# Kernel tuning notes

Hardware: AMD Instinct MI355X
Metric: run time of the kernel (lower is better)

## Reference

```python
import jax, jax.numpy as jnp
import numpy as np

T, B, V, E, H, L = 128, 32, 50000, 512, 512, 2


def _lstm_layer(x, h0, c0, Wih, Whh, bih, bhh):
    # x: [T, B, in]; torch gate order i, f, g, o
    def step(carry, xt):
        h, c = carry
        gates = xt @ Wih.T + bih + h @ Whh.T + bhh  # [B, 4H]
        i, f, g, o = jnp.split(gates, 4, axis=-1)
        c = jax.nn.sigmoid(f) * c + jax.nn.sigmoid(i) * jnp.tanh(g)
        h = jax.nn.sigmoid(o) * jnp.tanh(c)
        return (h, c), h
    (h, c), ys = jax.lax.scan(step, (h0, c0), x)
    return ys, h, c


def setup_inputs() -> dict:
    key = jax.random.key(0)
    ks = jax.random.split(key, 12)
    s = 0.02
    return {
        'word': jax.random.randint(ks[0], (B,), 0, V),
        'seq': jax.random.randint(ks[1], (T, B), 0, V),
        'emb': jax.random.normal(ks[2], (V, E), jnp.float32) * s,
        'w2h_W': jax.random.normal(ks[3], (H, E), jnp.float32) * s,
        'w2h_b': jnp.zeros((H,), jnp.float32),
        'Wih0': jax.random.normal(ks[4], (4 * H, E), jnp.float32) * s,
        'Whh0': jax.random.normal(ks[5], (4 * H, H), jnp.float32) * s,
        'bih0': jnp.zeros((4 * H,), jnp.float32),
        'bhh0': jnp.zeros((4 * H,), jnp.float32),
        'Wih1': jax.random.normal(ks[6], (4 * H, H), jnp.float32) * s,
        'Whh1': jax.random.normal(ks[7], (4 * H, H), jnp.float32) * s,
        'bih1': jnp.zeros((4 * H,), jnp.float32),
        'bhh1': jnp.zeros((4 * H,), jnp.float32),
        'dec_W': jax.random.normal(ks[8], (V, H), jnp.float32) * s,
        'dec_b': jnp.zeros((V,), jnp.float32),
    }


def reference(word, seq, emb, w2h_W, w2h_b, Wih0, Whh0, bih0, bhh0,
              Wih1, Whh1, bih1, bhh1, dec_W, dec_b):
    word_emb = emb[word]                       # [B, E]
    seq_emb = emb[seq]                         # [T, B, E] (dropouts are 0/eval)
    # init_hidden: c0 = word2hidden(word_emb) expanded to all layers, h0 = 0
    c0 = word_emb @ w2h_W.T + w2h_b            # [B, H]
    h0 = jnp.zeros_like(c0)
    # 2-layer LSTM; stepping all layers per timestep == running layers sequentially
    y0, h_f0, c_f0 = _lstm_layer(seq_emb, h0, c0, Wih0, Whh0, bih0, bhh0)
    y1, h_f1, c_f1 = _lstm_layer(y0, h0, c0, Wih1, Whh1, bih1, bhh1)
    out = y1.reshape(T * B, H)                 # [T*B, H]
    decoded = out @ dec_W.T + dec_b            # [T*B, V]
    h_final = jnp.stack([h_f0, h_f1], axis=0)  # [L, B, H]
    c_final = jnp.stack([c_f0, c_f1], axis=0)
    return decoded, h_final, c_final
```

## Files before the change

### kernel.cpp

```cpp
#include <hip/hip_runtime.h>
#include <hip/hip_bf16.h>
#include <cstdint>

#define T_STEPS 128
#define BATCH   32
#define VOCAB   50000
#define EDIM    512
#define HDIM    512
#define GDIM    2048
#define MROWS   4096
#define VPAD    50048

typedef short bf16x8 __attribute__((ext_vector_type(8)));
typedef float f32x4  __attribute__((ext_vector_type(4)));
typedef unsigned short us4 __attribute__((ext_vector_type(4)));
typedef unsigned short us8 __attribute__((ext_vector_type(8)));

#define MFMA16(a, b, c) __builtin_amdgcn_mfma_f32_16x16x32_bf16(a, b, c, 0, 0, 0)

__device__ __forceinline__ float fsigmoid(float x) {
    return 1.0f / (1.0f + __expf(-x));
}
__device__ __forceinline__ float ftanh(float x) {
    return 1.0f - 2.0f / (1.0f + __expf(2.0f * x));
}

__device__ __forceinline__ unsigned short f2bf(float f) {
    unsigned int u = __float_as_uint(f);
    u = (u + 0x7fffu + ((u >> 16) & 1u)) >> 16;
    return (unsigned short)u;
}


__global__ __launch_bounds__(256) void conv_decw(const float* __restrict__ src,
                                                 unsigned short* __restrict__ dst) {
    long i = ((long)blockIdx.x * 256 + threadIdx.x) * 8;
    if (i >= (long)VPAD * EDIM) return;
    long row = i >> 9;
    us8 v;
    if (row < VOCAB) {
        float4 a = *(const float4*)(src + i);
        float4 b = *(const float4*)(src + i + 4);
        v[0] = f2bf(a.x); v[1] = f2bf(a.y); v[2] = f2bf(a.z); v[3] = f2bf(a.w);
        v[4] = f2bf(b.x); v[5] = f2bf(b.y); v[6] = f2bf(b.z); v[7] = f2bf(b.w);
    } else {
        v = (us8)0;
    }
    *(us8*)(dst + i) = v;
}

__global__ __launch_bounds__(64) void pack_conv(const float* __restrict__ src,
                                                unsigned short* __restrict__ dst) {
    const int n = blockIdx.x;
    const int orig = (n & 3) * 512 + (n >> 2);
    const int k = threadIdx.x * 8;
    const float* s = src + (long)orig * 512 + k;
    float4 a = *(const float4*)s;
    float4 b = *(const float4*)(s + 4);
    us8 v;
    v[0] = f2bf(a.x); v[1] = f2bf(a.y); v[2] = f2bf(a.z); v[3] = f2bf(a.w);
    v[4] = f2bf(b.x); v[5] = f2bf(b.y); v[6] = f2bf(b.z); v[7] = f2bf(b.w);
    *(us8*)(dst + (long)n * 512 + k) = v;
}

__global__ __launch_bounds__(256) void pack_bias(const float* __restrict__ bih0,
                                                 const float* __restrict__ bhh0,
                                                 const float* __restrict__ bih1,
                                                 const float* __restrict__ bhh1,
                                                 float* __restrict__ b0p,
                                                 float* __restrict__ b1p) {
    const int n = blockIdx.x * 256 + threadIdx.x;
    const int orig = (n & 3) * 512 + (n >> 2);
    b0p[n] = bih0[orig] + bhh0[orig];
    b1p[n] = bih1[orig] + bhh1[orig];
}

__global__ __launch_bounds__(256) void gather_x(const int* __restrict__ seq,
                                                const float* __restrict__ emb,
                                                unsigned short* __restrict__ Xbf) {
    long i = ((long)blockIdx.x * 256 + threadIdx.x) * 4;
    if (i >= (long)MROWS * EDIM) return;
    int r   = (int)(i >> 9);
    int col = (int)(i & 511);
    const float* er = emb + (long)seq[r] * EDIM + col;
    float4 e = *(const float4*)er;
    us4 v;
    v[0] = f2bf(e.x); v[1] = f2bf(e.y); v[2] = f2bf(e.z); v[3] = f2bf(e.w);
    *(us4*)(Xbf + i) = v;
}

__global__ __launch_bounds__(256) void init_c0(const int* __restrict__ word,
                                               const float* __restrict__ emb,
                                               const float* __restrict__ w2hW,
                                               const float* __restrict__ w2hb,
                                               float* __restrict__ c0s, float* __restrict__ c1s,
                                               unsigned short* __restrict__ h0A,
                                               unsigned short* __restrict__ h1A) {
    const int idx = blockIdx.x * 256 + threadIdx.x;
    const int b = idx >> 9, hh = idx & 511;
    const float* er = emb + (long)word[b] * EDIM;
    const float* wr = w2hW + (long)hh * EDIM;
    float acc = w2hb[hh];
    #pragma unroll 4
    for (int k = 0; k < EDIM; k += 4) {
        float4 e4 = *(const float4*)(er + k);
        float4 w4 = *(const float4*)(wr + k);
        acc += e4.x * w4.x + e4.y * w4.y + e4.z * w4.z + e4.w * w4.w;
    }
    c0s[idx] = acc;
    c1s[idx] = acc;
    h0A[idx] = 0;
    h1A[idx] = 0;
}

__global__ __launch_bounds__(256) void gemm_bt128(const unsigned short* __restrict__ A,
                                                  const unsigned short* __restrict__ Bt,
                                                  float* __restrict__ C,
                                                  const float* __restrict__ bias1,
                                                  const float* __restrict__ bias2,
                                                  int K, int Nreal, long ldc, int ntn,
                                                  int mode) {
    __shared__ __align__(16) unsigned short As[128 * 64];
    __shared__ __align__(16) unsigned short Bs[128 * 64];
    const int tid  = threadIdx.x;
    long m0, n0;
    if (mode & 2) {
        m0 = (long)(blockIdx.x & 31) * 128;
        n0 = (long)(blockIdx.x >> 5) * 128;
    } else {
        m0 = (long)(blockIdx.x / ntn) * 128;
        n0 = (long)(blockIdx.x % ntn) * 128;
    }
    const int lane = tid & 63;
    const int wave = tid >> 6;
    const int wr = wave >> 1, wc = wave & 1;
    const int fr = lane & 15, fq = lane >> 4;

    f32x4 acc[4][4];
    #pragma unroll
    for (int i = 0; i < 4; ++i)
        #pragma unroll
        for (int j = 0; j < 4; ++j) acc[i][j] = (f32x4)0.0f;

    const int srow = tid >> 3;
    const int scol = (tid & 7) * 8;

    for (int kt = 0; kt < K; kt += 64) {
        #pragma unroll
        for (int i = 0; i < 4; ++i) {
            const unsigned short* ga = A  + (m0 + i * 32 + srow) * K + kt + scol;
            const unsigned short* gb = Bt + (n0 + i * 32 + srow) * K + kt + scol;
            __builtin_amdgcn_global_load_lds((const __attribute__((address_space(1))) void*)ga,
                                             (__attribute__((address_space(3))) void*)(As + i * 2048 + tid * 8),
                                             16, 0, 0);
            __builtin_amdgcn_global_load_lds((const __attribute__((address_space(1))) void*)gb,
                                             (__attribute__((address_space(3))) void*)(Bs + i * 2048 + tid * 8),
                                             16, 0, 0);
        }
        asm volatile("s_waitcnt vmcnt(0)" ::: "memory");
        __syncthreads();
        #pragma unroll
        for (int ks = 0; ks < 64; ks += 32) {
            bf16x8 af[4], bfr[4];
            #pragma unroll
            for (int mi = 0; mi < 4; ++mi)
                af[mi] = *(const bf16x8*)&As[(wr * 64 + mi * 16 + fr) * 64 + ks + fq * 8];
            #pragma unroll
            for (int ni = 0; ni < 4; ++ni)
                bfr[ni] = *(const bf16x8*)&Bs[(wc * 64 + ni * 16 + fr) * 64 + ks + fq * 8];
            #pragma unroll
            for (int mi = 0; mi < 4; ++mi)
                #pragma unroll
                for (int ni = 0; ni < 4; ++ni)
                    acc[mi][ni] = MFMA16(af[mi], bfr[ni], acc[mi][ni]);
        }
        __syncthreads();
    }

    #pragma unroll
    for (int mi = 0; mi < 4; ++mi) {
        const long row = m0 + wr * 64 + mi * 16 + fq * 4;
        #pragma unroll
        for (int ni = 0; ni < 4; ++ni) {
            const long col = n0 + wc * 64 + ni * 16 + fr;
            if (col < Nreal) {
                float bs = (bias1 ? bias1[col] : 0.0f) + (bias2 ? bias2[col] : 0.0f);
                #pragma unroll
                for (int r = 0; r < 4; ++r) {
                    float v = acc[mi][ni][r] + bs;
                    float* p = &C[(row + r) * ldc + col];
                    if (mode & 1) __builtin_nontemporal_store(v, p);
                    else *p = v;
                }
            }
        }
    }
}

__global__ __launch_bounds__(512) void lstm_step2(
        const float* __restrict__ G0,
        const unsigned short* __restrict__ Whh0p,
        const unsigned short* __restrict__ Wih1p,
        const unsigned short* __restrict__ Whh1p,
        const float* __restrict__ b1p,
        unsigned short* __restrict__ y0bf,
        unsigned short* __restrict__ y1bf,
        unsigned short* __restrict__ h0A, unsigned short* __restrict__ h0B,
        float* __restrict__ c0s,
        unsigned short* __restrict__ h1A, unsigned short* __restrict__ h1B,
        float* __restrict__ c1s,
        float* __restrict__ hf,
        int t) {
    __shared__ float part[8][32][32];
    int bid = blockIdx.x;
    const int tid  = threadIdx.x;
    const int wv   = tid >> 6, lane = tid & 63;
    const int fr   = lane & 15, fq = lane >> 4;

    int layer, tt, cg;
    if (bid < 64) { layer = 0; tt = t;     if (tt >= T_STEPS) return; cg = bid; }
    else          { layer = 1; tt = t - 1; if (tt < 0) return;       cg = bid - 64; }

    const unsigned short* hin;
    unsigned short* hout;
    float* cs;
    if (layer == 0) { hin = (tt & 1) ? h0B : h0A; hout = (tt & 1) ? h0A : h0B; cs = c0s; }
    else            { hin = (tt & 1) ? h1B : h1A; hout = (tt & 1) ? h1A : h1B; cs = c1s; }

    const int n_base = cg * 32;

    const int pb = tid >> 3, pu = tid & 7;
    const int si = pb * HDIM + cg * 8 + pu;
    float creg = 0.0f;
    float4 ad = make_float4(0.f, 0.f, 0.f, 0.f);
    if (tid < 256) {
        creg = cs[si];
        if (layer == 0) ad = *(const float4*)(G0 + ((long)tt * BATCH + pb) * GDIM + n_base + pu * 4);
        else            ad = *(const float4*)(b1p + n_base + pu * 4);
    }

    f32x4 acc[2][2];
    acc[0][0] = (f32x4)0.0f; acc[0][1] = (f32x4)0.0f;
    acc[1][0] = (f32x4)0.0f; acc[1][1] = (f32x4)0.0f;

    if (layer == 0) {
        const int kbase = wv * 64;
        const unsigned short* A0 = hin + fr * 512 + kbase + fq * 8;
        const unsigned short* A1 = A0 + 16 * 512;
        const unsigned short* B0 = Whh0p + (long)(n_base + fr) * 512 + kbase + fq * 8;
        const unsigned short* B1 = B0 + 16 * 512;
        #pragma unroll
        for (int i = 0; i < 2; ++i) {
            bf16x8 a0 = *(const bf16x8*)(A0 + i * 32);
            bf16x8 a1 = *(const bf16x8*)(A1 + i * 32);
            bf16x8 b0 = *(const bf16x8*)(B0 + i * 32);
            bf16x8 b1 = *(const bf16x8*)(B1 + i * 32);
            acc[0][0] = MFMA16(a0, b0, acc[0][0]);
            acc[0][1] = MFMA16(a0, b1, acc[0][1]);
            acc[1][0] = MFMA16(a1, b0, acc[1][0]);
            acc[1][1] = MFMA16(a1, b1, acc[1][1]);
        }
    } else {
        const unsigned short* Aop = (wv < 4) ? (y0bf + (long)tt * (BATCH * HDIM)) : hin;
        const unsigned short* Bop = (wv < 4) ? Wih1p : Whh1p;
        const int kbase = (wv & 3) * 128;
        const unsigned short* A0 = Aop + fr * 512 + kbase + fq * 8;
        const unsigned short* A1 = A0 + 16 * 512;
        const unsigned short* B0 = Bop + (long)(n_base + fr) * 512 + kbase + fq * 8;
        const unsigned short* B1 = B0 + 16 * 512;
        #pragma unroll
        for (int i = 0; i < 4; ++i) {
            bf16x8 a0 = *(const bf16x8*)(A0 + i * 32);
            bf16x8 a1 = *(const bf16x8*)(A1 + i * 32);
            bf16x8 b0 = *(const bf16x8*)(B0 + i * 32);
            bf16x8 b1 = *(const bf16x8*)(B1 + i * 32);
            acc[0][0] = MFMA16(a0, b0, acc[0][0]);
            acc[0][1] = MFMA16(a0, b1, acc[0][1]);
            acc[1][0] = MFMA16(a1, b0, acc[1][0]);
            acc[1][1] = MFMA16(a1, b1, acc[1][1]);
        }
    }

    #pragma unroll
    for (int mi = 0; mi < 2; ++mi)
        #pragma unroll
        for (int ni = 0; ni < 2; ++ni)
            #pragma unroll
            for (int r = 0; r < 4; ++r)
                part[wv][mi * 16 + fq * 4 + r][ni * 16 + fr] = acc[mi][ni][r];
    __syncthreads();

    if (tid < 256) {
        float4 g4 = *(const float4*)&part[0][pb][pu * 4];
        #pragma unroll
        for (int w = 1; w < 8; ++w) {
            float4 p4 = *(const float4*)&part[w][pb][pu * 4];
            g4.x += p4.x; g4.y += p4.y; g4.z += p4.z; g4.w += p4.w;
        }
        const float vi = g4.x + ad.x, vf = g4.y + ad.y;
        const float vg = g4.z + ad.z, vo = g4.w + ad.w;
        float c = fsigmoid(vf) * creg + fsigmoid(vi) * ftanh(vg);
        float h = fsigmoid(vo) * ftanh(c);
        cs[si] = c;
        const unsigned short hb = f2bf(h);
        hout[si] = hb;
        if (layer == 0) y0bf[(long)tt * (BATCH * HDIM) + si] = hb;
        else            y1bf[(long)tt * (BATCH * HDIM) + si] = hb;
        if (tt == T_STEPS - 1) hf[layer * (BATCH * HDIM) + si] = h;
    }
}

__global__ __launch_bounds__(256) void finalize_states(const float* __restrict__ hf,
                                                       const float* __restrict__ c0s,
                                                       const float* __restrict__ c1s,
                                                       float* __restrict__ out) {
    const int idx = blockIdx.x * 256 + threadIdx.x;
    const long base = (long)MROWS * VOCAB;
    float v;
    if (idx < 32768)      v = hf[idx];
    else if (idx < 49152) v = c0s[idx - 32768];
    else                  v = c1s[idx - 49152];
    out[base + idx] = v;
}

extern "C" void kernel_launch(void* const* d_in, const int* in_sizes, int n_in,
                              void* d_out, int out_size, void* d_ws, size_t ws_size,
                              hipStream_t stream) {
    const int*   word  = (const int*)d_in[0];
    const int*   seq   = (const int*)d_in[1];
    const float* emb   = (const float*)d_in[2];
    const float* w2hW  = (const float*)d_in[3];
    const float* w2hb  = (const float*)d_in[4];
    const float* Wih0  = (const float*)d_in[5];
    const float* Whh0  = (const float*)d_in[6];
    const float* bih0  = (const float*)d_in[7];
    const float* bhh0  = (const float*)d_in[8];
    const float* Wih1  = (const float*)d_in[9];
    const float* Whh1  = (const float*)d_in[10];
    const float* bih1  = (const float*)d_in[11];
    const float* bhh1  = (const float*)d_in[12];
    const float* dec_W = (const float*)d_in[13];
    const float* dec_b = (const float*)d_in[14];
    float* out = (float*)d_out;

    char* ws = (char*)d_ws;
    size_t off = 0;
    float*          G0    = (float*)(ws + off);          off += (size_t)MROWS * GDIM * 4;
    unsigned short* Xbf   = (unsigned short*)(ws + off); off += (size_t)MROWS * EDIM * 2;
    unsigned short* Wih0p = (unsigned short*)(ws + off); off += (size_t)GDIM  * EDIM * 2;
    unsigned short* Whh0p = (unsigned short*)(ws + off); off += (size_t)GDIM  * HDIM * 2;
    unsigned short* Wih1p = (unsigned short*)(ws + off); off += (size_t)GDIM  * HDIM * 2;
    unsigned short* Whh1p = (unsigned short*)(ws + off); off += (size_t)GDIM  * HDIM * 2;
    unsigned short* decWb = (unsigned short*)(ws + off); off += (size_t)VPAD  * EDIM * 2;
    unsigned short* y0bf  = (unsigned short*)(ws + off); off += (size_t)MROWS * HDIM * 2;
    unsigned short* y1bf  = (unsigned short*)(ws + off); off += (size_t)MROWS * HDIM * 2;
    float* b0p = (float*)(ws + off); off += (size_t)GDIM * 4;
    float* b1p = (float*)(ws + off); off += (size_t)GDIM * 4;
    unsigned short* h0A = (unsigned short*)(ws + off); off += (size_t)BATCH * HDIM * 2;
    unsigned short* h0B = (unsigned short*)(ws + off); off += (size_t)BATCH * HDIM * 2;
    unsigned short* h1A = (unsigned short*)(ws + off); off += (size_t)BATCH * HDIM * 2;
    unsigned short* h1B = (unsigned short*)(ws + off); off += (size_t)BATCH * HDIM * 2;
    float* c0s = (float*)(ws + off); off += (size_t)BATCH * HDIM * 4;
    float* c1s = (float*)(ws + off); off += (size_t)BATCH * HDIM * 4;
    float* hf  = (float*)(ws + off); off += (size_t)2 * BATCH * HDIM * 4;

    conv_decw<<<12512, 256, 0, stream>>>(dec_W, decWb);
    pack_conv<<<2048, 64, 0, stream>>>(Wih0, Wih0p);
    pack_conv<<<2048, 64, 0, stream>>>(Whh0, Whh0p);
    pack_conv<<<2048, 64, 0, stream>>>(Wih1, Wih1p);
    pack_conv<<<2048, 64, 0, stream>>>(Whh1, Whh1p);
    pack_bias<<<8, 256, 0, stream>>>(bih0, bhh0, bih1, bhh1, b0p, b1p);
    gather_x<<<2048, 256, 0, stream>>>(seq, emb, Xbf);
    init_c0<<<64, 256, 0, stream>>>(word, emb, w2hW, w2hb, c0s, c1s, h0A, h1A);

    gemm_bt128<<<32 * 16, 256, 0, stream>>>(Xbf, Wih0p, G0, b0p, nullptr,
                                            512, GDIM, (long)GDIM, 16, 0);

    for (int t = 0; t <= T_STEPS; ++t)
        lstm_step2<<<128, 512, 0, stream>>>(G0, Whh0p, Wih1p, Whh1p, b1p,
                                            y0bf, y1bf, h0A, h0B, c0s,
                                            h1A, h1B, c1s, hf, t);

    gemm_bt128<<<32 * 391, 256, 0, stream>>>(y1bf, decWb, out, dec_b, nullptr,
                                             512, VOCAB, (long)VOCAB, 391, 3);

    finalize_states<<<256, 256, 0, stream>>>(hf, c0s, c1s, out);
}
```

Before: 1.509 ms.

## Stage GEMM output through LDS for coalesced stores; store hidden state once into y buffers

The GEMM epilogue now writes each accumulator tile into shared memory and then stores full 128-column rows as float4 vectors. Before, each lane did strided scalar stores, and the decoder used nontemporal stores with an M-fastest block order. The LSTM step drops the separate ping-pong h buffers and reads and writes hidden state directly in the y0/y1 sequence buffers, which are shifted by one timestep. This removes a duplicate store per step. The risks are extra LDS traffic and syncs in the epilogue, a different block raster order for the decoder GEMM, and the loss of nontemporal stores on the large output.

```diff
diff --git a/kernel.cpp b/kernel.cpp
--- a/kernel.cpp
+++ b/kernel.cpp
@@ -10,6 +10,7 @@
 #define GDIM    2048
 #define MROWS   4096
 #define VPAD    50048
+#define BH      (BATCH * HDIM)
 
 typedef short bf16x8 __attribute__((ext_vector_type(8)));
 typedef float f32x4  __attribute__((ext_vector_type(4)));
@@ -94,8 +95,8 @@
                                                const float* __restrict__ w2hW,
                                                const float* __restrict__ w2hb,
                                                float* __restrict__ c0s, float* __restrict__ c1s,
-                                               unsigned short* __restrict__ h0A,
-                                               unsigned short* __restrict__ h1A) {
+                                               unsigned short* __restrict__ y0bf,
+                                               unsigned short* __restrict__ y1bf) {
     const int idx = blockIdx.x * 256 + threadIdx.x;
     const int b = idx >> 9, hh = idx & 511;
     const float* er = emb + (long)word[b] * EDIM;
@@ -109,8 +110,8 @@
     }
     c0s[idx] = acc;
     c1s[idx] = acc;
-    h0A[idx] = 0;
-    h1A[idx] = 0;
+    y0bf[idx] = 0;
+    y1bf[idx] = 0;
 }
 
 __global__ __launch_bounds__(256) void gemm_bt128(const unsigned short* __restrict__ A,
@@ -118,19 +119,15 @@
                                                   float* __restrict__ C,
                                                   const float* __restrict__ bias1,
                                                   const float* __restrict__ bias2,
-                                                  int K, int Nreal, long ldc, int ntn,
-                                                  int mode) {
-    __shared__ __align__(16) unsigned short As[128 * 64];
-    __shared__ __align__(16) unsigned short Bs[128 * 64];
+                                                  int K, int Nreal, long ldc, int ntn) {
+    __shared__ __align__(16) unsigned char smem[34048];
+    unsigned short* As = (unsigned short*)smem;
+    unsigned short* Bs = (unsigned short*)(smem + 16384);
+    float* ctile = (float*)smem;
+
     const int tid  = threadIdx.x;
-    long m0, n0;
-    if (mode & 2) {
-        m0 = (long)(blockIdx.x & 31) * 128;
-        n0 = (long)(blockIdx.x >> 5) * 128;
-    } else {
-        m0 = (long)(blockIdx.x / ntn) * 128;
-        n0 = (long)(blockIdx.x % ntn) * 128;
-    }
+    const long m0  = (long)(blockIdx.x / ntn) * 128;
+    const long n0  = (long)(blockIdx.x % ntn) * 128;
     const int lane = tid & 63;
     const int wave = tid >> 6;
     const int wr = wave >> 1, wc = wave & 1;
@@ -178,22 +175,34 @@
     }
 
     #pragma unroll
-    for (int mi = 0; mi < 4; ++mi) {
-        const long row = m0 + wr * 64 + mi * 16 + fq * 4;
-        #pragma unroll
-        for (int ni = 0; ni < 4; ++ni) {
-            const long col = n0 + wc * 64 + ni * 16 + fr;
-            if (col < Nreal) {
-                float bs = (bias1 ? bias1[col] : 0.0f) + (bias2 ? bias2[col] : 0.0f);
+    for (int h = 0; h < 2; ++h) {
+        if (wr == h) {
+            #pragma unroll
+            for (int ni = 0; ni < 4; ++ni) {
+                const long col = n0 + wc * 64 + ni * 16 + fr;
+                float bs = 0.0f;
+                if (col < Nreal)
+                    bs = (bias1 ? bias1[col] : 0.0f) + (bias2 ? bias2[col] : 0.0f);
                 #pragma unroll
-                for (int r = 0; r < 4; ++r) {
-                    float v = acc[mi][ni][r] + bs;
-                    float* p = &C[(row + r) * ldc + col];
-                    if (mode & 1) __builtin_nontemporal_store(v, p);
-                    else *p = v;
-                }
+                for (int mi = 0; mi < 4; ++mi)
+                    #pragma unroll
+                    for (int r = 0; r < 4; ++r)
+                        ctile[(mi * 16 + fq * 4 + r) * 132 + wc * 64 + ni * 16 + fr] =
+                            acc[mi][ni][r] + bs;
             }
         }
+        __syncthreads();
+        #pragma unroll
+        for (int j = 0; j < 8; ++j) {
+            const int flat = tid + j * 256;
+            const int row = flat >> 5, colq = flat & 31;
+            const long col4 = n0 + colq * 4;
+            if (col4 < Nreal) {
+                f32x4 v = *(const f32x4*)&ctile[row * 132 + colq * 4];
+                *(f32x4*)&C[(m0 + h * 64 + row) * ldc + col4] = v;
+            }
+        }
+        __syncthreads();
     }
 }
 
@@ -205,10 +214,7 @@
         const float* __restrict__ b1p,
         unsigned short* __restrict__ y0bf,
         unsigned short* __restrict__ y1bf,
-        unsigned short* __restrict__ h0A, unsigned short* __restrict__ h0B,
-        float* __restrict__ c0s,
-        unsigned short* __restrict__ h1A, unsigned short* __restrict__ h1B,
-        float* __restrict__ c1s,
+        float* __restrict__ c0s, float* __restrict__ c1s,
         float* __restrict__ hf,
         int t) {
     __shared__ float part[8][32][32];
@@ -222,10 +228,10 @@
     else          { layer = 1; tt = t - 1; if (tt < 0) return;       cg = bid - 64; }
 
     const unsigned short* hin;
-    unsigned short* hout;
+    unsigned short* yout;
     float* cs;
-    if (layer == 0) { hin = (tt & 1) ? h0B : h0A; hout = (tt & 1) ? h0A : h0B; cs = c0s; }
-    else            { hin = (tt & 1) ? h1B : h1A; hout = (tt & 1) ? h1A : h1B; cs = c1s; }
+    if (layer == 0) { hin = y0bf + (long)tt * BH; yout = y0bf + (long)(tt + 1) * BH; cs = c0s; }
+    else            { hin = y1bf + (long)tt * BH; yout = y1bf + (long)(tt + 1) * BH; cs = c1s; }
 
     const int n_base = cg * 32;
 
@@ -261,7 +267,7 @@
             acc[1][1] = MFMA16(a1, b1, acc[1][1]);
         }
     } else {
-        const unsigned short* Aop = (wv < 4) ? (y0bf + (long)tt * (BATCH * HDIM)) : hin;
+        const unsigned short* Aop = (wv < 4) ? (y0bf + (long)(tt + 1) * BH) : hin;
         const unsigned short* Bop = (wv < 4) ? Wih1p : Whh1p;
         const int kbase = (wv & 3) * 128;
         const unsigned short* A0 = Aop + fr * 512 + kbase + fq * 8;
@@ -302,11 +308,8 @@
         float c = fsigmoid(vf) * creg + fsigmoid(vi) * ftanh(vg);
         float h = fsigmoid(vo) * ftanh(c);
         cs[si] = c;
-        const unsigned short hb = f2bf(h);
-        hout[si] = hb;
-        if (layer == 0) y0bf[(long)tt * (BATCH * HDIM) + si] = hb;
-        else            y1bf[(long)tt * (BATCH * HDIM) + si] = hb;
-        if (tt == T_STEPS - 1) hf[layer * (BATCH * HDIM) + si] = h;
+        yout[si] = f2bf(h);
+        if (tt == T_STEPS - 1) hf[layer * BH + si] = h;
     }
 }
 
@@ -352,17 +355,13 @@
     unsigned short* Wih1p = (unsigned short*)(ws + off); off += (size_t)GDIM  * HDIM * 2;
     unsigned short* Whh1p = (unsigned short*)(ws + off); off += (size_t)GDIM  * HDIM * 2;
     unsigned short* decWb = (unsigned short*)(ws + off); off += (size_t)VPAD  * EDIM * 2;
-    unsigned short* y0bf  = (unsigned short*)(ws + off); off += (size_t)MROWS * HDIM * 2;
-    unsigned short* y1bf  = (unsigned short*)(ws + off); off += (size_t)MROWS * HDIM * 2;
+    unsigned short* y0bf  = (unsigned short*)(ws + off); off += (size_t)(T_STEPS + 1) * BH * 2;
+    unsigned short* y1bf  = (unsigned short*)(ws + off); off += (size_t)(T_STEPS + 1) * BH * 2;
     float* b0p = (float*)(ws + off); off += (size_t)GDIM * 4;
     float* b1p = (float*)(ws + off); off += (size_t)GDIM * 4;
-    unsigned short* h0A = (unsigned short*)(ws + off); off += (size_t)BATCH * HDIM * 2;
-    unsigned short* h0B = (unsigned short*)(ws + off); off += (size_t)BATCH * HDIM * 2;
-    unsigned short* h1A = (unsigned short*)(ws + off); off += (size_t)BATCH * HDIM * 2;
-    unsigned short* h1B = (unsigned short*)(ws + off); off += (size_t)BATCH * HDIM * 2;
-    float* c0s = (float*)(ws + off); off += (size_t)BATCH * HDIM * 4;
-    float* c1s = (float*)(ws + off); off += (size_t)BATCH * HDIM * 4;
-    float* hf  = (float*)(ws + off); off += (size_t)2 * BATCH * HDIM * 4;
+    float* c0s = (float*)(ws + off); off += (size_t)BH * 4;
+    float* c1s = (float*)(ws + off); off += (size_t)BH * 4;
+    float* hf  = (float*)(ws + off); off += (size_t)2 * BH * 4;
 
     conv_decw<<<12512, 256, 0, stream>>>(dec_W, decWb);
     pack_conv<<<2048, 64, 0, stream>>>(Wih0, Wih0p);
@@ -371,18 +370,17 @@
     pack_conv<<<2048, 64, 0, stream>>>(Whh1, Whh1p);
     pack_bias<<<8, 256, 0, stream>>>(bih0, bhh0, bih1, bhh1, b0p, b1p);
     gather_x<<<2048, 256, 0, stream>>>(seq, emb, Xbf);
-    init_c0<<<64, 256, 0, stream>>>(word, emb, w2hW, w2hb, c0s, c1s, h0A, h1A);
+    init_c0<<<64, 256, 0, stream>>>(word, emb, w2hW, w2hb, c0s, c1s, y0bf, y1bf);
 
     gemm_bt128<<<32 * 16, 256, 0, stream>>>(Xbf, Wih0p, G0, b0p, nullptr,
-                                            512, GDIM, (long)GDIM, 16, 0);
+                                            512, GDIM, (long)GDIM, 16);
 
     for (int t = 0; t <= T_STEPS; ++t)
         lstm_step2<<<128, 512, 0, stream>>>(G0, Whh0p, Wih1p, Whh1p, b1p,
-                                            y0bf, y1bf, h0A, h0B, c0s,
-                                            h1A, h1B, c1s, hf, t);
-
-    gemm_bt128<<<32 * 391, 256, 0, stream>>>(y1bf, decWb, out, dec_b, nullptr,
-                                             512, VOCAB, (long)VOCAB, 391, 3);
+                                            y0bf, y1bf, c0s, c1s, hf, t);
+
+    gemm_bt128<<<32 * 391, 256, 0, stream>>>(y1bf + BH, decWb, out, dec_b, nullptr,
+                                             512, VOCAB, (long)VOCAB, 391);
 
     finalize_states<<<256, 256, 0, stream>>>(hf, c0s, c1s, out);
 }
```

Measured after the change: 1.359 ms. 9.9% less time.
